# Kernel tuning notes

Hardware: AMD Instinct MI355X
Metric: run time of the kernel (lower is better)

Reference implementation:

```python
import jax, jax.numpy as jnp
import numpy as np

N_EMBD = 768
N_HEAD = 12

def setup_inputs() -> dict:
    key = jax.random.key(0)
    k_x, k_wa, k_ba, k_wp, k_bp = jax.random.split(key, 5)
    C = N_EMBD
    scale = 1.0 / np.sqrt(C)
    return {
        "x": jax.random.normal(k_x, (2, 4096, C), dtype=jnp.float32),
        "W_attn": jax.random.normal(k_wa, (C, 3 * C), dtype=jnp.float32) * scale,
        "b_attn": jax.random.normal(k_ba, (3 * C,), dtype=jnp.float32) * 0.01,
        "W_proj": jax.random.normal(k_wp, (C, C), dtype=jnp.float32) * scale,
        "b_proj": jax.random.normal(k_bp, (C,), dtype=jnp.float32) * 0.01,
    }

def reference(x, W_attn, b_attn, W_proj, b_proj) -> jnp.ndarray:
    B, T, C = x.shape
    H = N_HEAD
    D = C // H  # head dim
    qkv = x @ W_attn + b_attn                     # [B,T,3C]
    q, k, v = jnp.split(qkv, 3, axis=-1)
    # [B,T,C] -> [B,H,T,D]
    q = q.reshape(B, T, H, D).transpose(0, 2, 1, 3)
    k = k.reshape(B, T, H, D).transpose(0, 2, 1, 3)
    v = v.reshape(B, T, H, D).transpose(0, 2, 1, 3)
    scores = jnp.einsum("bhqd,bhkd->bhqk", q, k) * (1.0 / jnp.sqrt(jnp.float32(D)))
    attn = jax.nn.softmax(scores, axis=-1)        # dropout p=0.0 -> identity
    y = jnp.einsum("bhqk,bhkd->bhqd", attn, v)    # [B,H,T,D]
    y = y.transpose(0, 2, 1, 3).reshape(B, T, C)
    return y @ W_proj + b_proj
```

## Files before the change

kernel.cpp:

```cpp
#include <hip/hip_runtime.h>
#include <stdint.h>

#define NB 2
#define NT 4096
#define NC 768
#define NH 12
#define ND 64
#define NBT (NB*NT)
#define NQKV (3*NC)

typedef _Float16 half_t;
typedef __attribute__((ext_vector_type(8))) _Float16 f16x8;
typedef __attribute__((ext_vector_type(4))) _Float16 f16x4;
typedef __attribute__((ext_vector_type(2))) __fp16 fp16x2;
typedef __attribute__((ext_vector_type(4))) float f32x4;

#define MFMA16(a,b,c) __builtin_amdgcn_mfma_f32_16x16x32_f16((a),(b),(c),0,0,0)

__device__ __forceinline__ void load_lds16(const void* g, void* l) {
    auto gp = reinterpret_cast<__attribute__((address_space(1))) char*>(reinterpret_cast<uintptr_t>(g));
    auto lp = reinterpret_cast<__attribute__((address_space(3))) char*>(reinterpret_cast<uintptr_t>(l));
    __builtin_amdgcn_global_load_lds(gp, lp, 16, 0, 0);
}

#define PACK_BLKS ((NBT * NC / 4) / 256)
#define WA_TILES ((NC / 32) * (NQKV / 32))
#define WP_TILES ((NC / 32) * (NC / 32))
#define PREP_BLKS (PACK_BLKS + WA_TILES + WP_TILES)

__global__ __launch_bounds__(256) void k_prep(const float* __restrict__ x, half_t* __restrict__ xh,
                                              const float* __restrict__ Wa, half_t* __restrict__ Wat,
                                              const float* __restrict__ Wp, half_t* __restrict__ Wpt) {
    const int bid = blockIdx.x, tid = threadIdx.x;
    if (bid < PACK_BLKS) {
        const int i = bid * 256 + tid;
        float4 f = reinterpret_cast<const float4*>(x)[i];
        f16x4 h;
        h[0] = (half_t)f.x; h[1] = (half_t)f.y; h[2] = (half_t)f.z; h[3] = (half_t)f.w;
        reinterpret_cast<f16x4*>(xh)[i] = h;
        return;
    }
    __shared__ half_t tile[32][36];
    const float* in; half_t* out; int N, kt, nt;
    if (bid < PACK_BLKS + WA_TILES) {
        const int t = bid - PACK_BLKS;
        in = Wa; out = Wat; N = NQKV;
        kt = t / (NQKV / 32); nt = t - kt * (NQKV / 32);
    } else {
        const int t = bid - PACK_BLKS - WA_TILES;
        in = Wp; out = Wpt; N = NC;
        kt = t / (NC / 32); nt = t - kt * (NC / 32);
    }
    const int k0 = kt * 32, n0 = nt * 32;
    {
        const int r = tid >> 3, c = (tid & 7) * 4;
        float4 f = *reinterpret_cast<const float4*>(&in[(size_t)(k0 + r) * N + n0 + c]);
        tile[r][c] = (half_t)f.x; tile[r][c + 1] = (half_t)f.y;
        tile[r][c + 2] = (half_t)f.z; tile[r][c + 3] = (half_t)f.w;
    }
    __syncthreads();
    {
        const int rn = tid >> 3, ck = (tid & 7) * 4;
        f16x4 u;
        u[0] = tile[ck][rn]; u[1] = tile[ck + 1][rn];
        u[2] = tile[ck + 2][rn]; u[3] = tile[ck + 3][rn];
        *reinterpret_cast<f16x4*>(&out[(size_t)(n0 + rn) * NC + k0 + ck]) = u;
    }
}

__global__ __launch_bounds__(256, 3) void k_gemm0(const half_t* __restrict__ A, const half_t* __restrict__ Bt,
                                                  const float* __restrict__ bias, half_t* __restrict__ out,
                                                  half_t* __restrict__ Vt) {
    __shared__ half_t As[2][128 * 32];
    __shared__ half_t Bs[2][192 * 32];
    const int tid = threadIdx.x;
    const int lane = tid & 63, w = tid >> 6;
    const int m0 = blockIdx.x * 128, n0 = blockIdx.y * 192;
    const int wm = (w >> 1) * 64, wn = (w & 1) * 96;
    const int lr = lane & 15, lk = (lane >> 4) * 8;

    f32x4 acc[4][6];
#pragma unroll
    for (int a = 0; a < 4; ++a)
#pragma unroll
        for (int bq = 0; bq < 6; ++bq) acc[a][bq] = (f32x4){0.f, 0.f, 0.f, 0.f};

    const int ldsbase = (tid & ~63) * 16;
    const half_t* Arow = A  + (size_t)(m0 + (tid >> 2)) * NC + (tid & 3) * 8;
    const half_t* Brow = Bt + (size_t)(n0 + (tid >> 2)) * NC + (tid & 3) * 8;

    auto stage = [&](int buf, int k0) {
        load_lds16(Arow + k0,                    (char*)&As[buf][0] + ldsbase);
        load_lds16(Arow + (size_t)64 * NC + k0,  (char*)&As[buf][0] + 4096 + ldsbase);
        load_lds16(Brow + k0,                    (char*)&Bs[buf][0] + ldsbase);
        load_lds16(Brow + (size_t)64 * NC + k0,  (char*)&Bs[buf][0] + 4096 + ldsbase);
        load_lds16(Brow + (size_t)128 * NC + k0, (char*)&Bs[buf][0] + 8192 + ldsbase);
    };

    stage(0, 0);
    __syncthreads();
    int cur = 0;

    for (int ks = 0; ks < 24; ++ks) {
        if (ks < 23) stage(cur ^ 1, (ks + 1) * 32);
        f16x8 af[4];
#pragma unroll
        for (int mi = 0; mi < 4; ++mi)
            af[mi] = *reinterpret_cast<const f16x8*>(&As[cur][(wm + mi * 16 + lr) * 32 + lk]);
#pragma unroll
        for (int ni = 0; ni < 6; ++ni) {
            f16x8 bf = *reinterpret_cast<const f16x8*>(&Bs[cur][(wn + ni * 16 + lr) * 32 + lk]);
#pragma unroll
            for (int mi = 0; mi < 4; ++mi)
                acc[mi][ni] = MFMA16(af[mi], bf, acc[mi][ni]);
        }
        __syncthreads();
        cur ^= 1;
    }

    const int rg = (lane >> 4) * 4;

    if (n0 >= 2 * NC) {
        half_t* q = (w < 2) ? (half_t*)((char*)&As[0][0] + w * 8192)
                            : (half_t*)((char*)&Bs[0][0] + (w - 2) * 8192);
        const int M0 = m0 + wm;
        const int bb = M0 >> 12;
        const int trow = M0 & (NT - 1);
#pragma unroll
        for (int p = 0; p < 2; ++p) {
#pragma unroll
            for (int n3 = 0; n3 < 3; ++n3) {
                const int ni = p * 3 + n3;
                const int c = n3 * 16 + lr;
                const float bv = bias[n0 + wn + p * 48 + c];
                const int xsw = (c & 7) << 3;
#pragma unroll
                for (int mi = 0; mi < 4; ++mi) {
                    const int t0 = mi * 16 + rg;
                    union { f16x4 v; fp16x2 hh[2]; } o;
                    o.hh[0] = __builtin_amdgcn_cvt_pkrtz(acc[mi][ni][0] + bv, acc[mi][ni][1] + bv);
                    o.hh[1] = __builtin_amdgcn_cvt_pkrtz(acc[mi][ni][2] + bv, acc[mi][ni][3] + bv);
                    *reinterpret_cast<f16x4*>(&q[c * 64 + (t0 ^ xsw)]) = o.v;
                }
            }
#pragma unroll
            for (int j = 0; j < 6; ++j) {
                const int cl = j * 8 + (lane >> 3);
                const int tt = (lane & 7) * 8;
                f16x8 val = *reinterpret_cast<const f16x8*>(&q[cl * 64 + (tt ^ ((cl & 7) << 3))]);
                const int dcol = n0 - 2 * NC + wn + p * 48 + cl;
                const int bh = bb * NH + (dcol >> 6);
                *reinterpret_cast<f16x8*>(&Vt[((size_t)bh * ND + (dcol & 63)) * NT + trow + tt]) = val;
            }
        }
        return;
    }

#pragma unroll
    for (int ni = 0; ni < 6; ++ni) {
        const int gn = n0 + wn + ni * 16 + lr;
        const float bv = bias[gn];
#pragma unroll
        for (int mi = 0; mi < 4; ++mi)
#pragma unroll
            for (int i = 0; i < 4; ++i) {
                const size_t gm = (size_t)(m0 + wm + mi * 16 + rg + i);
                out[gm * NQKV + gn] = (half_t)(acc[mi][ni][i] + bv);
            }
    }
}

__global__ __launch_bounds__(256) void k_gemm1(const half_t* __restrict__ A, const half_t* __restrict__ Bt,
                                               const float* __restrict__ bias, float* __restrict__ out) {
    __shared__ half_t As[2][128 * 32];
    __shared__ half_t Bs[2][128 * 32];
    const int tid = threadIdx.x;
    const int lane = tid & 63, w = tid >> 6;
    const int m0 = blockIdx.x * 128, n0 = blockIdx.y * 96;
    const int wm = (w >> 1) * 64, wn = (w & 1) * 48;
    const int lr = lane & 15, lk = (lane >> 4) * 8;

    f32x4 acc[4][3];
#pragma unroll
    for (int a = 0; a < 4; ++a)
#pragma unroll
        for (int bq = 0; bq < 3; ++bq) acc[a][bq] = (f32x4){0.f, 0.f, 0.f, 0.f};

    const int ldsbase = (tid & ~63) * 16;
    const half_t* Arow = A  + (size_t)(m0 + (tid >> 2)) * NC + (tid & 3) * 8;
    const half_t* Brow = Bt + (size_t)(n0 + (tid >> 2)) * NC + (tid & 3) * 8;

    auto stage = [&](int buf, int k0) {
        load_lds16(Arow + k0,                   (char*)&As[buf][0] + ldsbase);
        load_lds16(Arow + (size_t)64 * NC + k0, (char*)&As[buf][0] + 4096 + ldsbase);
        load_lds16(Brow + k0,                   (char*)&Bs[buf][0] + ldsbase);
        load_lds16(Brow + (size_t)64 * NC + k0, (char*)&Bs[buf][0] + 4096 + ldsbase);
    };

    stage(0, 0);
    __syncthreads();
    int cur = 0;

    for (int ks = 0; ks < 24; ++ks) {
        if (ks < 23) stage(cur ^ 1, (ks + 1) * 32);
        f16x8 af[4], bf[3];
#pragma unroll
        for (int mi = 0; mi < 4; ++mi)
            af[mi] = *reinterpret_cast<const f16x8*>(&As[cur][(wm + mi * 16 + lr) * 32 + lk]);
#pragma unroll
        for (int ni = 0; ni < 3; ++ni)
            bf[ni] = *reinterpret_cast<const f16x8*>(&Bs[cur][(wn + ni * 16 + lr) * 32 + lk]);
#pragma unroll
        for (int mi = 0; mi < 4; ++mi)
#pragma unroll
            for (int ni = 0; ni < 3; ++ni)
                acc[mi][ni] = MFMA16(af[mi], bf[ni], acc[mi][ni]);
        __syncthreads();
        cur ^= 1;
    }

    const int rg = (lane >> 4) * 4;
#pragma unroll
    for (int ni = 0; ni < 3; ++ni) {
        const int gn = n0 + wn + ni * 16 + lr;
        const float bv = bias[gn];
#pragma unroll
        for (int mi = 0; mi < 4; ++mi)
#pragma unroll
            for (int i = 0; i < 4; ++i) {
                const size_t gm = (size_t)(m0 + wm + mi * 16 + rg + i);
                out[gm * NC + gn] = acc[mi][ni][i] + bv;
            }
    }
}

struct __align__(16) AttnSmem {
    union {
        struct { half_t K[2][64 * 64]; half_t V[2][64 * 64]; } m;
        struct { float y[2][64][64]; float l[2][64][4]; } r;
    };
};

__global__ __launch_bounds__(256, 3) void k_attn(const half_t* __restrict__ qkv, const half_t* __restrict__ Vt,
                                                 half_t* __restrict__ Y) {
    __shared__ AttnSmem sm;
    const int tid = threadIdx.x, lane = tid & 63, w = tid >> 6;
    const int qw = w & 1, kw = w >> 1;
    const int lr = lane & 15, g = lane >> 4;
    const int qt = blockIdx.x, bh = blockIdx.y;
    const int b = bh / NH, h = bh - b * NH;
    const half_t* Qp = qkv + (size_t)b * NT * NQKV + h * ND;
    const half_t* Kp = Qp + NC;
    const half_t* Vbase = Vt + (size_t)bh * ND * NT;
    const int q0 = qt * 128 + qw * 64;

    const int sr = tid >> 3;
    const int colh = (((tid & 7) << 3)) ^ ((sr & 7) << 3);
    const int wub = (tid & ~63) * 16;

    f16x8 aq[4][2];
    const half_t cch = (half_t)(0.125f * 1.4426950408889634f);
#pragma unroll
    for (int qf = 0; qf < 4; ++qf)
#pragma unroll
        for (int dh = 0; dh < 2; ++dh) {
            aq[qf][dh] = *reinterpret_cast<const f16x8*>(&Qp[(size_t)(q0 + qf * 16 + lr) * NQKV + dh * 32 + g * 8]);
#pragma unroll
            for (int j = 0; j < 8; ++j) aq[qf][dh][j] = aq[qf][dh][j] * cch;
        }

    const int swk = (lr & 7) << 3;
    const int cA = (g * 8) ^ swk;
    const int cB = (32 + g * 8) ^ swk;
    const int psw = lr & 7;
    const int goff = (g & 1) << 2;
    const int vcol[2] = { (((g >> 1) + 4 * kw + 0) ^ psw) * 8 + goff,
                          (((g >> 1) + 4 * kw + 2) ^ psw) * 8 + goff };

    f32x4 y[4][4];
#pragma unroll
    for (int qf = 0; qf < 4; ++qf)
#pragma unroll
        for (int df = 0; df < 4; ++df) y[qf][df] = (f32x4){0.f, 0.f, 0.f, 0.f};
    float l_[4] = {0.f, 0.f, 0.f, 0.f};

    auto stagebuf = [&](int buf, const half_t* Ks, const half_t* Vs) {
        char* kdst = (char*)&sm.m.K[buf][0] + wub;
        char* vdst = (char*)&sm.m.V[buf][0] + wub;
        load_lds16(Ks, kdst);
        load_lds16(Ks + (size_t)32 * NQKV, kdst + 4096);
        load_lds16(Vs, vdst);
        load_lds16(Vs + (size_t)32 * NT, vdst + 4096);
    };

    const half_t* ksrc = Kp + (size_t)sr * NQKV + colh;
    const half_t* vsrc = Vbase + (size_t)sr * NT + colh;
    stagebuf(0, ksrc, vsrc);
    ksrc += (size_t)64 * NQKV;
    vsrc += 64;
    __syncthreads();
    int cur = 0;
    const int stb = 2 * kw;

    for (int t = 0; t < NT / 64; ++t) {
        if (t < NT / 64 - 1) {
            stagebuf(cur ^ 1, ksrc, vsrc);
            ksrc += (size_t)64 * NQKV;
            vsrc += 64;
        }

        f32x4 s[4][2];
#pragma unroll
        for (int qf = 0; qf < 4; ++qf) { s[qf][0] = (f32x4){0.f,0.f,0.f,0.f}; s[qf][1] = (f32x4){0.f,0.f,0.f,0.f}; }
        const half_t* Kc = &sm.m.K[cur][0];
        __builtin_amdgcn_s_setprio(1);
#pragma unroll
        for (int sl = 0; sl < 2; ++sl) {
            const int row = (stb + sl) * 16 + lr;
            f16x8 bk0 = *reinterpret_cast<const f16x8*>(&Kc[row * 64 + cA]);
            s[0][sl] = MFMA16(bk0, aq[0][0], s[0][sl]);
            s[1][sl] = MFMA16(bk0, aq[1][0], s[1][sl]);
            s[2][sl] = MFMA16(bk0, aq[2][0], s[2][sl]);
            s[3][sl] = MFMA16(bk0, aq[3][0], s[3][sl]);
            f16x8 bk1 = *reinterpret_cast<const f16x8*>(&Kc[row * 64 + cB]);
            s[0][sl] = MFMA16(bk1, aq[0][1], s[0][sl]);
            s[1][sl] = MFMA16(bk1, aq[1][1], s[1][sl]);
            s[2][sl] = MFMA16(bk1, aq[2][1], s[2][sl]);
            s[3][sl] = MFMA16(bk1, aq[3][1], s[3][sl]);
        }
        __builtin_amdgcn_s_setprio(0);

        f16x8 pb[4];
#pragma unroll
        for (int qf = 0; qf < 4; ++qf) {
            float ps = 0.f;
            union { f16x8 v; fp16x2 h[4]; } u;
#pragma unroll
            for (int hs = 0; hs < 2; ++hs) {
                const float p0 = __builtin_amdgcn_exp2f(s[qf][hs][0]);
                const float p1 = __builtin_amdgcn_exp2f(s[qf][hs][1]);
                const float p2 = __builtin_amdgcn_exp2f(s[qf][hs][2]);
                const float p3 = __builtin_amdgcn_exp2f(s[qf][hs][3]);
                u.h[2 * hs]     = __builtin_amdgcn_cvt_pkrtz(p0, p1);
                u.h[2 * hs + 1] = __builtin_amdgcn_cvt_pkrtz(p2, p3);
                ps += (p0 + p1) + (p2 + p3);
            }
            pb[qf] = u.v;
            l_[qf] += ps;
        }

        const half_t* Vc = &sm.m.V[cur][0];
        __builtin_amdgcn_s_setprio(1);
#pragma unroll
        for (int df = 0; df < 4; ++df) {
            const half_t* vrow = &Vc[(df * 16 + lr) * 64];
            union { f16x8 v; f16x4 q[2]; } va;
            va.q[0] = *reinterpret_cast<const f16x4*>(vrow + vcol[0]);
            va.q[1] = *reinterpret_cast<const f16x4*>(vrow + vcol[1]);
            y[0][df] = MFMA16(va.v, pb[0], y[0][df]);
            y[1][df] = MFMA16(va.v, pb[1], y[1][df]);
            y[2][df] = MFMA16(va.v, pb[2], y[2][df]);
            y[3][df] = MFMA16(va.v, pb[3], y[3][df]);
        }
        __builtin_amdgcn_s_setprio(0);

        __syncthreads();
        cur ^= 1;
    }

    if (kw == 1) {
#pragma unroll
        for (int qf = 0; qf < 4; ++qf)
#pragma unroll
            for (int df = 0; df < 4; ++df) {
                const int jb = (qf * 16 + df * 4) ^ ((lane & 7) << 2);
                *reinterpret_cast<f32x4*>(&sm.r.y[qw][lane][jb]) = y[qf][df];
            }
#pragma unroll
        for (int qf = 0; qf < 4; ++qf) sm.r.l[qw][lane][qf] = l_[qf];
    }
    __syncthreads();
    if (kw == 0) {
#pragma unroll
        for (int qf = 0; qf < 4; ++qf) {
#pragma unroll
            for (int df = 0; df < 4; ++df) {
                const int jb = (qf * 16 + df * 4) ^ ((lane & 7) << 2);
                const f32x4 yp = *reinterpret_cast<const f32x4*>(&sm.r.y[qw][lane][jb]);
                y[qf][df] += yp;
            }
            float l = l_[qf] + sm.r.l[qw][lane][qf];
            l += __shfl_xor(l, 16);
            l += __shfl_xor(l, 32);
            const float rl = 1.f / l;
            half_t* Yp = Y + (size_t)(b * NT + q0 + qf * 16 + lr) * NC + h * ND + g * 4;
#pragma unroll
            for (int df = 0; df < 4; ++df) {
                union { f16x4 v; fp16x2 hh[2]; } o;
                o.hh[0] = __builtin_amdgcn_cvt_pkrtz(y[qf][df][0] * rl, y[qf][df][1] * rl);
                o.hh[1] = __builtin_amdgcn_cvt_pkrtz(y[qf][df][2] * rl, y[qf][df][3] * rl);
                *reinterpret_cast<f16x4*>(Yp + df * 16) = o.v;
            }
        }
    }
}

extern "C" void kernel_launch(void* const* d_in, const int* in_sizes, int n_in,
                              void* d_out, int out_size, void* d_ws, size_t ws_size,
                              hipStream_t stream) {
    const float* x  = (const float*)d_in[0];
    const float* Wa = (const float*)d_in[1];
    const float* ba = (const float*)d_in[2];
    const float* Wp = (const float*)d_in[3];
    const float* bp = (const float*)d_in[4];
    float* out = (float*)d_out;

    char* ws = (char*)d_ws;
    half_t* xh   = (half_t*)ws; ws += (size_t)NBT * NC * 2;
    half_t* Wat  = (half_t*)ws; ws += (size_t)NQKV * NC * 2;
    half_t* Wpt  = (half_t*)ws; ws += (size_t)NC * NC * 2;
    half_t* qkvh = (half_t*)ws; ws += (size_t)NBT * NQKV * 2;
    half_t* vt   = (half_t*)ws; ws += (size_t)NB * NH * ND * NT * 2;
    half_t* yh   = (half_t*)ws; ws += (size_t)NBT * NC * 2;

    k_prep<<<PREP_BLKS, 256, 0, stream>>>(x, xh, Wa, Wat, Wp, Wpt);
    k_gemm0<<<dim3(NBT / 128, NQKV / 192), 256, 0, stream>>>(xh, Wat, ba, qkvh, vt);
    k_attn<<<dim3(NT / 128, NB * NH), 256, 0, stream>>>(qkvh, vt, yh);
    k_gemm1<<<dim3(NBT / 128, NC / 96), 256, 0, stream>>>(yh, Wpt, bp, out);
}
```

Measured before the change: 184.0 us.

## Switch attention kernel from 16x16x32 to 32x32x16 MFMA tiles

Rewrites the attention inner loop to use 32x32x16 f16 MFMA instructions in place of 16x16x32. Q fragments, K/V LDS access patterns, the softmax packing and the output epilogue are remapped to the 32-lane layout. The row-sum reduction now needs one cross-half shuffle instead of two. The larger tiles cut the number of MFMA issues and LDS fragment loads per tile, at the risk of different register pressure and LDS bank behaviour.

```diff
diff --git a/kernel.cpp b/kernel.cpp
--- a/kernel.cpp
+++ b/kernel.cpp
@@ -14,8 +14,10 @@
 typedef __attribute__((ext_vector_type(4))) _Float16 f16x4;
 typedef __attribute__((ext_vector_type(2))) __fp16 fp16x2;
 typedef __attribute__((ext_vector_type(4))) float f32x4;
+typedef __attribute__((ext_vector_type(16))) float f32x16;
 
 #define MFMA16(a,b,c) __builtin_amdgcn_mfma_f32_16x16x32_f16((a),(b),(c),0,0,0)
+#define MFMA32(a,b,c) __builtin_amdgcn_mfma_f32_32x32x16_f16((a),(b),(c),0,0,0)
 
 __device__ __forceinline__ void load_lds16(const void* g, void* l) {
     auto gp = reinterpret_cast<__attribute__((address_space(1))) char*>(reinterpret_cast<uintptr_t>(g));
@@ -246,7 +248,7 @@
     __shared__ AttnSmem sm;
     const int tid = threadIdx.x, lane = tid & 63, w = tid >> 6;
     const int qw = w & 1, kw = w >> 1;
-    const int lr = lane & 15, g = lane >> 4;
+    const int ln = lane & 31, lh = lane >> 5;
     const int qt = blockIdx.x, bh = blockIdx.y;
     const int b = bh / NH, h = bh - b * NH;
     const half_t* Qp = qkv + (size_t)b * NT * NQKV + h * ND;
@@ -258,31 +260,33 @@
     const int colh = (((tid & 7) << 3)) ^ ((sr & 7) << 3);
     const int wub = (tid & ~63) * 16;
 
-    f16x8 aq[4][2];
+    f16x8 aq[2][4];
     const half_t cch = (half_t)(0.125f * 1.4426950408889634f);
 #pragma unroll
-    for (int qf = 0; qf < 4; ++qf)
-#pragma unroll
-        for (int dh = 0; dh < 2; ++dh) {
-            aq[qf][dh] = *reinterpret_cast<const f16x8*>(&Qp[(size_t)(q0 + qf * 16 + lr) * NQKV + dh * 32 + g * 8]);
-#pragma unroll
-            for (int j = 0; j < 8; ++j) aq[qf][dh][j] = aq[qf][dh][j] * cch;
-        }
-
-    const int swk = (lr & 7) << 3;
-    const int cA = (g * 8) ^ swk;
-    const int cB = (32 + g * 8) ^ swk;
-    const int psw = lr & 7;
-    const int goff = (g & 1) << 2;
-    const int vcol[2] = { (((g >> 1) + 4 * kw + 0) ^ psw) * 8 + goff,
-                          (((g >> 1) + 4 * kw + 2) ^ psw) * 8 + goff };
-
-    f32x4 y[4][4];
-#pragma unroll
-    for (int qf = 0; qf < 4; ++qf)
-#pragma unroll
-        for (int df = 0; df < 4; ++df) y[qf][df] = (f32x4){0.f, 0.f, 0.f, 0.f};
-    float l_[4] = {0.f, 0.f, 0.f, 0.f};
+    for (int q2 = 0; q2 < 2; ++q2)
+#pragma unroll
+        for (int dk = 0; dk < 4; ++dk) {
+            aq[q2][dk] = *reinterpret_cast<const f16x8*>(&Qp[(size_t)(q0 + q2 * 32 + ln) * NQKV + dk * 16 + lh * 8]);
+#pragma unroll
+            for (int j = 0; j < 8; ++j) aq[q2][dk][j] = aq[q2][dk][j] * cch;
+        }
+
+    const int krow = kw * 32 + ln;
+    const int ksw = ln & 7;
+    int kcol[4];
+#pragma unroll
+    for (int dk = 0; dk < 4; ++dk) kcol[dk] = (((dk << 1) | lh) ^ ksw) << 3;
+
+    const int psw = ln & 7;
+    const int goff = lh * 4;
+    const int vcol[2][2] = { { ((kw * 4 + 0) ^ psw) * 8 + goff, ((kw * 4 + 1) ^ psw) * 8 + goff },
+                             { ((kw * 4 + 2) ^ psw) * 8 + goff, ((kw * 4 + 3) ^ psw) * 8 + goff } };
+
+    const f32x16 z16 = {0.f,0.f,0.f,0.f, 0.f,0.f,0.f,0.f, 0.f,0.f,0.f,0.f, 0.f,0.f,0.f,0.f};
+    f32x16 y_[2][2];
+#pragma unroll
+    for (int q2 = 0; q2 < 2; ++q2) { y_[q2][0] = z16; y_[q2][1] = z16; }
+    float l_[2] = {0.f, 0.f};
 
     auto stagebuf = [&](int buf, const half_t* Ks, const half_t* Vs) {
         char* kdst = (char*)&sm.m.K[buf][0] + wub;
@@ -300,7 +304,6 @@
     vsrc += 64;
     __syncthreads();
     int cur = 0;
-    const int stb = 2 * kw;
 
     for (int t = 0; t < NT / 64; ++t) {
         if (t < NT / 64 - 1) {
@@ -309,58 +312,50 @@
             vsrc += 64;
         }
 
-        f32x4 s[4][2];
-#pragma unroll
-        for (int qf = 0; qf < 4; ++qf) { s[qf][0] = (f32x4){0.f,0.f,0.f,0.f}; s[qf][1] = (f32x4){0.f,0.f,0.f,0.f}; }
+        f32x16 s_[2];
+        s_[0] = z16; s_[1] = z16;
         const half_t* Kc = &sm.m.K[cur][0];
         __builtin_amdgcn_s_setprio(1);
 #pragma unroll
-        for (int sl = 0; sl < 2; ++sl) {
-            const int row = (stb + sl) * 16 + lr;
-            f16x8 bk0 = *reinterpret_cast<const f16x8*>(&Kc[row * 64 + cA]);
-            s[0][sl] = MFMA16(bk0, aq[0][0], s[0][sl]);
-            s[1][sl] = MFMA16(bk0, aq[1][0], s[1][sl]);
-            s[2][sl] = MFMA16(bk0, aq[2][0], s[2][sl]);
-            s[3][sl] = MFMA16(bk0, aq[3][0], s[3][sl]);
-            f16x8 bk1 = *reinterpret_cast<const f16x8*>(&Kc[row * 64 + cB]);
-            s[0][sl] = MFMA16(bk1, aq[0][1], s[0][sl]);
-            s[1][sl] = MFMA16(bk1, aq[1][1], s[1][sl]);
-            s[2][sl] = MFMA16(bk1, aq[2][1], s[2][sl]);
-            s[3][sl] = MFMA16(bk1, aq[3][1], s[3][sl]);
+        for (int dk = 0; dk < 4; ++dk) {
+            f16x8 ak = *reinterpret_cast<const f16x8*>(&Kc[krow * 64 + kcol[dk]]);
+            s_[0] = MFMA32(ak, aq[0][dk], s_[0]);
+            s_[1] = MFMA32(ak, aq[1][dk], s_[1]);
         }
         __builtin_amdgcn_s_setprio(0);
 
-        f16x8 pb[4];
-#pragma unroll
-        for (int qf = 0; qf < 4; ++qf) {
+        f16x8 pb[2][2];
+#pragma unroll
+        for (int q2 = 0; q2 < 2; ++q2) {
             float ps = 0.f;
-            union { f16x8 v; fp16x2 h[4]; } u;
-#pragma unroll
-            for (int hs = 0; hs < 2; ++hs) {
-                const float p0 = __builtin_amdgcn_exp2f(s[qf][hs][0]);
-                const float p1 = __builtin_amdgcn_exp2f(s[qf][hs][1]);
-                const float p2 = __builtin_amdgcn_exp2f(s[qf][hs][2]);
-                const float p3 = __builtin_amdgcn_exp2f(s[qf][hs][3]);
-                u.h[2 * hs]     = __builtin_amdgcn_cvt_pkrtz(p0, p1);
-                u.h[2 * hs + 1] = __builtin_amdgcn_cvt_pkrtz(p2, p3);
-                ps += (p0 + p1) + (p2 + p3);
-            }
-            pb[qf] = u.v;
-            l_[qf] += ps;
+#pragma unroll
+            for (int ks2 = 0; ks2 < 2; ++ks2) {
+                union { f16x8 v; fp16x2 hh[4]; } u;
+#pragma unroll
+                for (int jp = 0; jp < 4; ++jp) {
+                    const float pa = __builtin_amdgcn_exp2f(s_[q2][ks2 * 8 + jp * 2]);
+                    const float pc = __builtin_amdgcn_exp2f(s_[q2][ks2 * 8 + jp * 2 + 1]);
+                    u.hh[jp] = __builtin_amdgcn_cvt_pkrtz(pa, pc);
+                    ps += pa + pc;
+                }
+                pb[q2][ks2] = u.v;
+            }
+            l_[q2] += ps;
         }
 
         const half_t* Vc = &sm.m.V[cur][0];
         __builtin_amdgcn_s_setprio(1);
 #pragma unroll
-        for (int df = 0; df < 4; ++df) {
-            const half_t* vrow = &Vc[(df * 16 + lr) * 64];
-            union { f16x8 v; f16x4 q[2]; } va;
-            va.q[0] = *reinterpret_cast<const f16x4*>(vrow + vcol[0]);
-            va.q[1] = *reinterpret_cast<const f16x4*>(vrow + vcol[1]);
-            y[0][df] = MFMA16(va.v, pb[0], y[0][df]);
-            y[1][df] = MFMA16(va.v, pb[1], y[1][df]);
-            y[2][df] = MFMA16(va.v, pb[2], y[2][df]);
-            y[3][df] = MFMA16(va.v, pb[3], y[3][df]);
+        for (int dt = 0; dt < 2; ++dt) {
+            const half_t* vrow = &Vc[(dt * 32 + ln) * 64];
+#pragma unroll
+            for (int ks2 = 0; ks2 < 2; ++ks2) {
+                union { f16x8 v; f16x4 q[2]; } va;
+                va.q[0] = *reinterpret_cast<const f16x4*>(vrow + vcol[ks2][0]);
+                va.q[1] = *reinterpret_cast<const f16x4*>(vrow + vcol[ks2][1]);
+                y_[0][dt] = MFMA32(va.v, pb[0][ks2], y_[0][dt]);
+                y_[1][dt] = MFMA32(va.v, pb[1][ks2], y_[1][dt]);
+            }
         }
         __builtin_amdgcn_s_setprio(0);
 
@@ -368,39 +363,47 @@
         cur ^= 1;
     }
 
+    l_[0] += __shfl_xor(l_[0], 32);
+    l_[1] += __shfl_xor(l_[1], 32);
+
     if (kw == 1) {
 #pragma unroll
-        for (int qf = 0; qf < 4; ++qf)
-#pragma unroll
-            for (int df = 0; df < 4; ++df) {
-                const int jb = (qf * 16 + df * 4) ^ ((lane & 7) << 2);
-                *reinterpret_cast<f32x4*>(&sm.r.y[qw][lane][jb]) = y[qf][df];
-            }
-#pragma unroll
-        for (int qf = 0; qf < 4; ++qf) sm.r.l[qw][lane][qf] = l_[qf];
+        for (int q2 = 0; q2 < 2; ++q2)
+#pragma unroll
+            for (int dt = 0; dt < 2; ++dt)
+#pragma unroll
+                for (int r = 0; r < 4; ++r) {
+                    const int c = q2 * 8 + dt * 4 + r;
+                    const int jb = (c * 4) ^ ((lane & 7) << 2);
+                    f32x4 tv;
+                    tv[0] = y_[q2][dt][4 * r];     tv[1] = y_[q2][dt][4 * r + 1];
+                    tv[2] = y_[q2][dt][4 * r + 2]; tv[3] = y_[q2][dt][4 * r + 3];
+                    *reinterpret_cast<f32x4*>(&sm.r.y[qw][lane][jb]) = tv;
+                }
+        sm.r.l[qw][lane][0] = l_[0];
+        sm.r.l[qw][lane][1] = l_[1];
     }
     __syncthreads();
     if (kw == 0) {
 #pragma unroll
-        for (int qf = 0; qf < 4; ++qf) {
-#pragma unroll
-            for (int df = 0; df < 4; ++df) {
-                const int jb = (qf * 16 + df * 4) ^ ((lane & 7) << 2);
-                const f32x4 yp = *reinterpret_cast<const f32x4*>(&sm.r.y[qw][lane][jb]);
-                y[qf][df] += yp;
-            }
-            float l = l_[qf] + sm.r.l[qw][lane][qf];
-            l += __shfl_xor(l, 16);
-            l += __shfl_xor(l, 32);
+        for (int q2 = 0; q2 < 2; ++q2) {
+            const float l = l_[q2] + sm.r.l[qw][lane][q2];
             const float rl = 1.f / l;
-            half_t* Yp = Y + (size_t)(b * NT + q0 + qf * 16 + lr) * NC + h * ND + g * 4;
-#pragma unroll
-            for (int df = 0; df < 4; ++df) {
-                union { f16x4 v; fp16x2 hh[2]; } o;
-                o.hh[0] = __builtin_amdgcn_cvt_pkrtz(y[qf][df][0] * rl, y[qf][df][1] * rl);
-                o.hh[1] = __builtin_amdgcn_cvt_pkrtz(y[qf][df][2] * rl, y[qf][df][3] * rl);
-                *reinterpret_cast<f16x4*>(Yp + df * 16) = o.v;
-            }
+            half_t* Yp = Y + (size_t)(b * NT + q0 + q2 * 32 + ln) * NC + h * ND;
+#pragma unroll
+            for (int dt = 0; dt < 2; ++dt)
+#pragma unroll
+                for (int r = 0; r < 4; ++r) {
+                    const int c = q2 * 8 + dt * 4 + r;
+                    const int jb = (c * 4) ^ ((lane & 7) << 2);
+                    const f32x4 yp = *reinterpret_cast<const f32x4*>(&sm.r.y[qw][lane][jb]);
+                    union { f16x4 v; fp16x2 hh[2]; } o;
+                    o.hh[0] = __builtin_amdgcn_cvt_pkrtz((y_[q2][dt][4 * r] + yp[0]) * rl,
+                                                         (y_[q2][dt][4 * r + 1] + yp[1]) * rl);
+                    o.hh[1] = __builtin_amdgcn_cvt_pkrtz((y_[q2][dt][4 * r + 2] + yp[2]) * rl,
+                                                         (y_[q2][dt][4 * r + 3] + yp[3]) * rl);
+                    *reinterpret_cast<f16x4*>(Yp + dt * 32 + 8 * r + 4 * lh) = o.v;
+                }
         }
     }
 }
```

After: 192.2 us. 4.5% more time.
